# Optimization experiments

Hardware: AMD Instinct MI355X
Metric: run time of the kernel (lower is better)

The kernel has to match this reference:

```python
import jax, jax.numpy as jnp
import numpy as np

B, T_ENC, T_DEC = 32, 600, 600
TARGET, PRE, HID, ATT, LOCF, LOCK, POSTH = 80, 256, 512, 128, 32, 31, 512


def _lstm(x, h, c, wih, whh, bih, bhh):
    g = x @ wih.T + bih + h @ whh.T + bhh
    i, f, gg, o = jnp.split(g, 4, axis=-1)
    c2 = jax.nn.sigmoid(f) * c + jax.nn.sigmoid(i) * jnp.tanh(gg)
    return jax.nn.sigmoid(o) * jnp.tanh(c2), c2


def _conv1d(x, w, pad):
    return jax.lax.conv_general_dilated(x, w, (1,), [(pad, pad)], dimension_numbers=('NCH', 'OIH', 'NCH'))


def setup_inputs():
    key = jax.random.key(0)
    ks = jax.random.split(key, 24)
    rn = lambda k, s: jax.random.normal(k, s, dtype=jnp.float32) * 0.05
    return {
        'encoder_inputs': jax.random.normal(ks[0], (B, T_ENC, HID), dtype=jnp.float32),
        'decoder_inputs': jax.random.normal(ks[1], (B, T_DEC, TARGET), dtype=jnp.float32),
        'pn_w1': rn(ks[2], (PRE, TARGET)), 'pn_b1': jnp.zeros((PRE,), jnp.float32),
        'pn_w2': rn(ks[3], (PRE, PRE)), 'pn_b2': jnp.zeros((PRE,), jnp.float32),
        'arnn_wih': rn(ks[4], (4 * HID, PRE + HID)), 'arnn_whh': rn(ks[5], (4 * HID, HID)),
        'arnn_bih': jnp.zeros((4 * HID,), jnp.float32), 'arnn_bhh': jnp.zeros((4 * HID,), jnp.float32),
        'drnn_wih': rn(ks[6], (4 * HID, 2 * HID)), 'drnn_whh': rn(ks[7], (4 * HID, HID)),
        'drnn_bih': jnp.zeros((4 * HID,), jnp.float32), 'drnn_bhh': jnp.zeros((4 * HID,), jnp.float32),
        'mem_w': rn(ks[8], (ATT, HID)), 'mem_b': jnp.zeros((ATT,), jnp.float32),
        'q_w': rn(ks[9], (ATT, HID)),
        'loc_conv_w': rn(ks[10], (LOCF, 2, LOCK)),
        'loc_fc_w': rn(ks[11], (ATT, LOCF)),
        'v_w': rn(ks[12], (1, ATT)),
        'proj_w': rn(ks[13], (TARGET, 2 * HID)),
        'post_w0': rn(ks[14], (POSTH, TARGET, 5)), 'post_b0': jnp.zeros((POSTH,), jnp.float32),
        'post_w1': rn(ks[15], (POSTH, POSTH, 5)), 'post_b1': jnp.zeros((POSTH,), jnp.float32),
        'post_w2': rn(ks[16], (POSTH, POSTH, 5)), 'post_b2': jnp.zeros((POSTH,), jnp.float32),
        'post_w3': rn(ks[17], (POSTH, POSTH, 5)), 'post_b3': jnp.zeros((POSTH,), jnp.float32),
        'post_w4': rn(ks[18], (TARGET, POSTH, 5)), 'post_b4': jnp.zeros((TARGET,), jnp.float32),
    }


def _forward(encoder_inputs, decoder_inputs, pn_w1, pn_b1, pn_w2, pn_b2,
             arnn_wih, arnn_whh, arnn_bih, arnn_bhh,
             drnn_wih, drnn_whh, drnn_bih, drnn_bhh,
             mem_w, mem_b, q_w, loc_conv_w, loc_fc_w, v_w, proj_w,
             post_w0, post_b0, post_w1, post_b1, post_w2, post_b2,
             post_w3, post_b3, post_w4, post_b4):
    Bsz, Tdec, tdim = decoder_inputs.shape
    Tenc = encoder_inputs.shape[1]
    dt = decoder_inputs.dtype
    # prenet on [go_frame; decoder_inputs]; loop consumes frames 0..Tdec-1
    go = jnp.zeros((Bsz, 1, tdim), dt)
    dec = jnp.concatenate([go, decoder_inputs], axis=1)
    pre = jax.nn.relu(jax.nn.relu(dec @ pn_w1.T + pn_b1) @ pn_w2.T + pn_b2)
    xs = jnp.transpose(pre[:, :Tdec], (1, 0, 2))  # (Tdec, B, PRE)
    proc_mem = encoder_inputs @ mem_w.T + mem_b  # (B, Tenc, ATT)
    z = jnp.zeros((Bsz, HID), dt)
    zw = jnp.zeros((Bsz, Tenc), dt)
    carry0 = (z, z, z, z, z, zw, zw)

    def step(carry, dec_in):
        ah, ac, dh, dc, ctx, w, wcum = carry
        ah, ac = _lstm(jnp.concatenate([dec_in, ctx], -1), ah, ac, arnn_wih, arnn_whh, arnn_bih, arnn_bhh)
        wcat = jnp.stack([w, wcum], axis=1)  # (B, 2, Tenc)
        loc = _conv1d(wcat, loc_conv_w, (LOCK - 1) // 2)  # (B, LOCF, Tenc)
        loc = jnp.einsum('bct,ac->bta', loc, loc_fc_w)  # (B, Tenc, ATT)
        q = ah @ q_w.T  # (B, ATT)
        e = jnp.tanh(q[:, None, :] + proc_mem + loc) @ v_w[0]  # (B, Tenc)
        w2 = jax.nn.softmax(e, axis=-1)
        ctx2 = jnp.einsum('bt,bte->be', w2, encoder_inputs)
        wcum2 = wcum + w2
        dh2, dc2 = _lstm(jnp.concatenate([ah, ctx2], -1), dh, dc, drnn_wih, drnn_whh, drnn_bih, drnn_bhh)
        mel = jnp.concatenate([dh2, ctx2], -1) @ proj_w.T  # (B, TARGET)
        return (ah, ac, dh2, dc2, ctx2, w2, wcum2), mel

    _, mels = jax.lax.scan(step, carry0, xs)
    mel_out = jnp.transpose(mels, (1, 0, 2))  # (B, Tdec, TARGET)
    # postnet: 5 conv1d layers, tanh on all but last (eval mode, no dropout)
    y = jnp.transpose(mel_out, (0, 2, 1))  # (B, TARGET, Tdec)
    y = jnp.tanh(_conv1d(y, post_w0, 2) + post_b0[None, :, None])
    y = jnp.tanh(_conv1d(y, post_w1, 2) + post_b1[None, :, None])
    y = jnp.tanh(_conv1d(y, post_w2, 2) + post_b2[None, :, None])
    y = jnp.tanh(_conv1d(y, post_w3, 2) + post_b3[None, :, None])
    y = _conv1d(y, post_w4, 2) + post_b4[None, :, None]  # (B, TARGET, Tdec)
    return mel_out + jnp.transpose(y, (0, 2, 1))


def reference(encoder_inputs, decoder_inputs, pn_w1, pn_b1, pn_w2, pn_b2,
              arnn_wih, arnn_whh, arnn_bih, arnn_bhh,
              drnn_wih, drnn_whh, drnn_bih, drnn_bhh,
              mem_w, mem_b, q_w, loc_conv_w, loc_fc_w, v_w, proj_w,
              post_w0, post_b0, post_w1, post_b1, post_w2, post_b2,
              post_w3, post_b3, post_w4, post_b4):
    return _forward(encoder_inputs, decoder_inputs, pn_w1, pn_b1, pn_w2, pn_b2,
                    arnn_wih, arnn_whh, arnn_bih, arnn_bhh,
                    drnn_wih, drnn_whh, drnn_bih, drnn_bhh,
                    mem_w, mem_b, q_w, loc_conv_w, loc_fc_w, v_w, proj_w,
                    post_w0, post_b0, post_w1, post_b1, post_w2, post_b2,
                    post_w3, post_b3, post_w4, post_b4)
```

## Files before the change

kernel.cpp:

```cpp
#include <hip/hip_runtime.h>
#include <hip/hip_bf16.h>

typedef __hip_bfloat16 bf16;

#define NB   32
#define TE   600
#define TD   600
#define TGT  80
#define PREN 256
#define HID  512
#define ATTD 128
#define LF   32
#define LK   31
#define PH   512

__device__ __forceinline__ float b2f(bf16 x){ return __bfloat162float(x); }

__device__ __forceinline__ void ld8bf(const bf16* p, float* o){
  const uint4 u = *(const uint4*)p;
  o[0]=__uint_as_float(u.x<<16); o[1]=__uint_as_float(u.x&0xFFFF0000u);
  o[2]=__uint_as_float(u.y<<16); o[3]=__uint_as_float(u.y&0xFFFF0000u);
  o[4]=__uint_as_float(u.z<<16); o[5]=__uint_as_float(u.z&0xFFFF0000u);
  o[6]=__uint_as_float(u.w<<16); o[7]=__uint_as_float(u.w&0xFFFF0000u);
}

__device__ __forceinline__ void ld8f(const float* p, float* o){
  float4 a=*(const float4*)p, b=*(const float4*)(p+4);
  o[0]=a.x;o[1]=a.y;o[2]=a.z;o[3]=a.w;
  o[4]=b.x;o[5]=b.y;o[6]=b.z;o[7]=b.w;
}

__device__ __forceinline__ float dot8(const float* w, const float* z){
  return w[0]*z[0]+w[1]*z[1]+w[2]*z[2]+w[3]*z[3]
       + w[4]*z[4]+w[5]*z[5]+w[6]*z[6]+w[7]*z[7];
}

__device__ __forceinline__ float sigm(float x){ return 1.f/(1.f+__expf(-x)); }
__device__ __forceinline__ float tanhfast(float x){
  float e = __expf(2.f*x);
  return 1.f - 2.f/(e+1.f);
}

__global__ __launch_bounds__(256) void k_prenet(const float* __restrict__ dec,
    const float* __restrict__ w1, const float* __restrict__ b1,
    const float* __restrict__ w2, const float* __restrict__ b2,
    bf16* __restrict__ XS)
{
  int t = blockIdx.x, tid = threadIdx.x;
  __shared__ __align__(16) float fr[NB*TGT];
  __shared__ __align__(16) float h1[NB*PREN];
  for (int i=tid;i<NB*TGT;i+=256){
    int b=i/TGT,c=i%TGT;
    fr[b*TGT+c] = (t==0)?0.f:dec[((size_t)b*TD+(t-1))*TGT+c];
  }
  __syncthreads();
  {
    int oc=tid; float bb=b1[oc];
    const float* wr = w1 + (size_t)oc*TGT;
    for (int b=0;b<NB;b++){
      float acc=bb;
      for (int k=0;k<TGT;k+=8){
        float wv[8]; ld8f(wr+k,wv);
        acc += dot8(wv, fr + b*TGT + k);
      }
      h1[b*PREN+oc]=fmaxf(acc,0.f);
    }
  }
  __syncthreads();
  {
    int oc=tid; float bb=b2[oc];
    const float* wr = w2 + (size_t)oc*PREN;
    for (int b=0;b<NB;b++){
      float acc=bb;
      for (int k=0;k<PREN;k+=8){
        float wv[8]; ld8f(wr+k,wv);
        acc += dot8(wv, h1 + b*PREN + k);
      }
      XS[((size_t)t*NB+b)*PREN+oc]=__float2bfloat16(fmaxf(acc,0.f));
    }
  }
}

__global__ __launch_bounds__(256) void k_procmem(const float* __restrict__ enc,
    const float* __restrict__ mw, const float* __restrict__ mb, bf16* __restrict__ PM)
{
  int t=blockIdx.x, tid=threadIdx.x;
  __shared__ __align__(16) float xe[16*HID];
  int a = tid & 127, bh = tid >> 7;
  float bb = mb[a];
  const float* wr = mw + (size_t)a*HID;
  for (int half=0; half<2; half++){
    __syncthreads();
    for (int i=tid;i<16*HID;i+=256){
      int bl=i>>9, h=i&511;
      xe[i] = enc[((size_t)(half*16+bl)*TE + t)*HID + h];
    }
    __syncthreads();
    for (int bl=bh*8; bl<bh*8+8; bl++){
      float acc=bb;
      for (int k=0;k<HID;k+=8){
        float wv[8]; ld8f(wr+k,wv);
        acc += dot8(wv, xe + bl*HID + k);
      }
      PM[((size_t)(half*16+bl)*TE + t)*ATTD + a] = __float2bfloat16(acc);
    }
  }
}

__global__ __launch_bounds__(256) void k_bc(
    const float* __restrict__ AH, const bf16* __restrict__ PML,
    const float* __restrict__ enc,
    const float* __restrict__ qw, const float* __restrict__ vw,
    float* __restrict__ W, float* __restrict__ WCUM, float* __restrict__ CTXw,
    const float* __restrict__ DHp, const float* __restrict__ CTXp,
    const float* __restrict__ projw, float* __restrict__ MEL, int t)
{
  int blk=blockIdx.x, tid=threadIdx.x;
  if (blk>=128){
    if (t==0) return;
    int b = blk-128;
    const float* dh = DHp + b*HID;
    const float* c2 = CTXp + b*HID;
    #pragma unroll
    for (int pass=0; pass<3; ++pass){
      int o = pass*32 + (tid>>3);
      if (o<TGT){
        int j = tid&7;
        const float* pw = projw + (size_t)o*1024;
        float a=0.f;
        for (int i=0;i<16;i++){
          int k = j*128 + i*8;
          const float* zp = (k<512)? dh+k : c2+(k-512);
          float z[8]; ld8f(zp,z);
          float wv[8]; ld8f(pw+k,wv);
          a += dot8(wv,z);
        }
        a += __shfl_xor(a,1); a += __shfl_xor(a,2); a += __shfl_xor(a,4);
        if (j==0) MEL[((size_t)b*TD + (t-1))*TGT + o] = a;
      }
    }
    return;
  }
  int b = blk>>2, k4 = blk&3;
  __shared__ float qs[128], vv[128];
  __shared__ __align__(16) float el[608], wl[608];
  __shared__ __align__(16) float4 part4[256];
  __shared__ float red[4];
  if (tid < 128){
    vv[tid] = vw[tid];
    const float* qr = qw + (size_t)tid*HID;
    const float* ah = AH + b*HID;
    float acc = 0.f;
    for (int kk=0;kk<HID;kk+=8){
      float wv2[8]; ld8f(qr+kk,wv2);
      acc += dot8(wv2, ah+kk);
    }
    qs[tid] = acc;
  }
  __syncthreads();
  for (int r=0;r<3;r++){
    int tt=tid+r*256;
    if (tt<TE){
      const uint4* pm4=(const uint4*)(PML+((size_t)b*TE+tt)*ATTD);
      float s=0.f;
      #pragma unroll 4
      for (int g=0;g<16;g++){
        uint4 um=pm4[g];
        unsigned mm[4]={um.x,um.y,um.z,um.w};
        #pragma unroll
        for (int q=0;q<4;q++){
          int a=g*8+q*2;
          float x0=qs[a]  +__uint_as_float(mm[q]<<16);
          float x1=qs[a+1]+__uint_as_float(mm[q]&0xFFFF0000u);
          s+=vv[a]*tanhfast(x0)+vv[a+1]*tanhfast(x1);
        }
      }
      el[tt]=s;
    }
  }
  __syncthreads();
  float e0[3]; float mx=-1e30f;
  #pragma unroll
  for (int r=0;r<3;r++){
    int i=tid+r*256;
    float v=(i<TE)? el[i] : -1e30f;
    e0[r]=v; mx=fmaxf(mx,v);
  }
  for (int off=1;off<64;off<<=1) mx=fmaxf(mx,__shfl_xor(mx,off));
  if ((tid&63)==0) red[tid>>6]=mx;
  __syncthreads();
  float m=fmaxf(fmaxf(red[0],red[1]),fmaxf(red[2],red[3]));
  float ex[3]; float s=0.f;
  #pragma unroll
  for (int r=0;r<3;r++){
    int i=tid+r*256;
    ex[r]=(i<TE)? __expf(e0[r]-m) : 0.f;
    s+=ex[r];
  }
  for (int off=1;off<64;off<<=1) s+=__shfl_xor(s,off);
  __syncthreads();
  if ((tid&63)==0) red[tid>>6]=s;
  __syncthreads();
  float inv=1.f/(red[0]+red[1]+red[2]+red[3]);
  #pragma unroll
  for (int r=0;r<3;r++){
    int i=tid+r*256;
    if (i<TE){
      float w2=ex[r]*inv;
      wl[i]=w2;
      if (k4==0){
        W[(size_t)b*TE+i]=w2;
        WCUM[(size_t)b*TE+i]+=w2;
      }
    }
  }
  __syncthreads();
  {
    int hl = tid&31, tl = tid>>5;
    int h = k4*128 + hl*4;
    const float4* ep4 = (const float4*)(enc + ((size_t)b*TE)*HID + h);
    float4 acc; acc.x=0.f; acc.y=0.f; acc.z=0.f; acc.w=0.f;
    for (int u=0; u<75; ++u){
      int tt = tl + u*8;
      float w = wl[tt];
      float4 e = ep4[(size_t)tt*(HID/4)];
      acc.x += w*e.x; acc.y += w*e.y; acc.z += w*e.z; acc.w += w*e.w;
    }
    part4[tid]=acc;
  }
  __syncthreads();
  if (tid<32){
    float4 s4; s4.x=0.f; s4.y=0.f; s4.z=0.f; s4.w=0.f;
    #pragma unroll
    for (int k=0;k<8;k++){
      float4 p = part4[k*32+tid];
      s4.x+=p.x; s4.y+=p.y; s4.z+=p.z; s4.w+=p.w;
    }
    *(float4*)(CTXw + b*HID + k4*128 + tid*4) = s4;
  }
}

__global__ __launch_bounds__(256) void k_ea(
    const bf16* __restrict__ XS,
    const float* __restrict__ CTXt, const float* __restrict__ AHt,
    float* __restrict__ AHw, float* __restrict__ AC,
    const float* __restrict__ DHp, float* __restrict__ DHw, float* __restrict__ DC,
    const float* __restrict__ W, const float* __restrict__ WCUM,
    const float* __restrict__ convw, const float* __restrict__ fcw,
    const bf16* __restrict__ PM, bf16* __restrict__ PML,
    const float* __restrict__ awih, const float* __restrict__ awhh,
    const float* __restrict__ abih, const float* __restrict__ abhh,
    const float* __restrict__ dwih, const float* __restrict__ dwhh,
    const float* __restrict__ dbih, const float* __restrict__ dbhh,
    int t)
{
  int blk=blockIdx.x, tid=threadIdx.x;
  if (blk<512){
    int s = t+1;
    if (s>=TD) return;
    int b=tid>>3, j=tid&7;
    int cell = blk;
    const bf16* xs = XS + ((size_t)s*NB+b)*PREN;
    const float* cx = CTXt + b*HID;
    const float* hr = AHt + b*HID;
    float acc[4];
    #pragma unroll
    for (int q=0;q<4;q++) acc[q]=0.f;
    for (int i=0;i<20;i++){
      int k8=i*64+j*8;
      float z[8];
      if (k8<256) ld8bf(xs+k8,z);
      else ld8f((k8<768)? cx+(k8-256) : hr+(k8-768), z);
      #pragma unroll
      for (int g=0;g<4;g++){
        int row = g*HID + cell;
        const float* wp = (k8<768) ? (awih + (size_t)row*768 + k8)
                                   : (awhh + (size_t)row*HID + (k8-768));
        float wv[8]; ld8f(wp,wv);
        acc[g] += dot8(wv,z);
      }
    }
    #pragma unroll
    for (int q=0;q<4;q++){
      acc[q] += __shfl_xor(acc[q],1);
      acc[q] += __shfl_xor(acc[q],2);
      acc[q] += __shfl_xor(acc[q],4);
    }
    if (j==0){
      float g0=acc[0]+abih[0*HID+cell]+abhh[0*HID+cell];
      float g1=acc[1]+abih[1*HID+cell]+abhh[1*HID+cell];
      float g2=acc[2]+abih[2*HID+cell]+abhh[2*HID+cell];
      float g3=acc[3]+abih[3*HID+cell]+abhh[3*HID+cell];
      float c2 = sigm(g1)*AC[b*HID+cell] + sigm(g0)*tanhfast(g2);
      AC[b*HID+cell]=c2;
      AHw[b*HID+cell]=sigm(g3)*tanhfast(c2);
    }
  } else if (blk<1024){
    if (t<0) return;
    int b=tid>>3, j=tid&7;
    int cell = blk-512;
    const float* ah  = AHt + b*HID;
    const float* cx  = CTXt + b*HID;
    const float* dhr = DHp + b*HID;
    float acc[4];
    #pragma unroll
    for (int q=0;q<4;q++) acc[q]=0.f;
    for (int i=0;i<24;i++){
      int k8=i*64+j*8;
      const float* zp = (k8<512)? ah+k8 : (k8<1024)? cx+(k8-512) : dhr+(k8-1024);
      float z[8]; ld8f(zp,z);
      #pragma unroll
      for (int g=0;g<4;g++){
        int row = g*HID + cell;
        const float* wp = (k8<1024) ? (dwih + (size_t)row*1024 + k8)
                                    : (dwhh + (size_t)row*HID + (k8-1024));
        float wv[8]; ld8f(wp,wv);
        acc[g] += dot8(wv,z);
      }
    }
    #pragma unroll
    for (int q=0;q<4;q++){
      acc[q] += __shfl_xor(acc[q],1);
      acc[q] += __shfl_xor(acc[q],2);
      acc[q] += __shfl_xor(acc[q],4);
    }
    if (j==0){
      float g0=acc[0]+dbih[0*HID+cell]+dbhh[0*HID+cell];
      float g1=acc[1]+dbih[1*HID+cell]+dbhh[1*HID+cell];
      float g2=acc[2]+dbih[2*HID+cell]+dbhh[2*HID+cell];
      float g3=acc[3]+dbih[3*HID+cell]+dbhh[3*HID+cell];
      float c2 = sigm(g1)*DC[b*HID+cell] + sigm(g0)*tanhfast(g2);
      DC[b*HID+cell]=c2;
      DHw[b*HID+cell]=sigm(g3)*tanhfast(c2);
    }
  } else {
    if (t+1>=TD) return;
    int idx = blk-1024;
    int b = idx>>3, s8 = idx&7;
    int tb = s8*75;
    __shared__ __align__(16) float wp_[112], wc_[112];
    __shared__ __align__(16) float cw0[32*31], cw1[32*31];
    __shared__ __align__(16) float cb[75*32];
    __shared__ __align__(16) float fcs[128*33];
    if (tid<105){
      int g = tb-15+tid;
      bool ok = (g>=0 && g<TE);
      wp_[tid] = ok ? W[(size_t)b*TE+g] : 0.f;
      wc_[tid] = ok ? WCUM[(size_t)b*TE+g] : 0.f;
    }
    for (int i=tid;i<32*31;i+=256){
      int c=i/31, k=i-c*31;
      cw0[i] = convw[c*62 + k];
      cw1[i] = convw[c*62 + 31 + k];
    }
    for (int i=tid;i<128*33;i+=256){
      int a=i/33, c=i-a*33;
      fcs[i] = (c<32)? fcw[a*32+c] : 0.f;
    }
    __syncthreads();
    for (int i=tid;i<75*32;i+=256){
      int tt=i>>5, c=i&31;
      float s=0.f;
      for (int k=0;k<LK;k++)
        s += cw0[c*31+k]*wp_[tt+k] + cw1[c*31+k]*wc_[tt+k];
      cb[tt*32+c]=s;
    }
    __syncthreads();
    {
      int lane = tid&63, tl = tid>>6;
      int a0 = 2*lane;
      for (int tt=tl; tt<75; tt+=4){
        float l0=0.f, l1=0.f;
        const float* cbr = cb + tt*32;
        #pragma unroll
        for (int c=0;c<32;c++){
          float cv = cbr[c];
          l0 += fcs[a0*33+c]*cv;
          l1 += fcs[(a0+1)*33+c]*cv;
        }
        size_t off = ((size_t)b*TE + tb + tt)*ATTD + a0;
        PML[off]   = __float2bfloat16(l0 + b2f(PM[off]));
        PML[off+1] = __float2bfloat16(l1 + b2f(PM[off+1]));
      }
    }
  }
}

__global__ __launch_bounds__(256) void k_melfinal(const float* __restrict__ DH,
    const float* __restrict__ CTX, const float* __restrict__ projw, float* __restrict__ MEL)
{
  int gid=blockIdx.x*256+threadIdx.x;
  if (gid>=NB*TGT) return;
  int o=gid%TGT, b=gid/TGT;
  const float* pw=projw+(size_t)o*1024;
  float a=0.f;
  for (int k=0;k<HID;k+=8){
    float wv[8]; ld8f(pw+k,wv);
    a += dot8(wv, DH + b*HID + k);
  }
  for (int k=0;k<HID;k+=8){
    float wv[8]; ld8f(pw+512+k,wv);
    a += dot8(wv, CTX + b*HID + k);
  }
  MEL[((size_t)b*TD+599)*TGT+o]=a;
}

__global__ __launch_bounds__(256) void k_conv(
    const void* __restrict__ inv_, bf16* __restrict__ out,
    const float* __restrict__ w, const float* __restrict__ bias,
    int IC, int OC, int mel_in, int do_tanh, int b0)
{
  __shared__ __align__(16) float xs[256*36];
  int bl=blockIdx.x, bg=b0+bl, oct=blockIdx.y, t0=blockIdx.z*32, tid=threadIdx.x;
  int oc = oct*256 + tid;
  float acc[32];
  #pragma unroll
  for (int q=0;q<32;q++) acc[q]=0.f;
  int nch=(IC+255)/256;
  const float* inf_ = (const float*)inv_;
  const bf16*  inb_ = (const bf16*)inv_;
  for (int ch=0;ch<nch;ch++){
    int icb=ch*256, icn=min(256,IC-icb);
    __syncthreads();
    for (int i=tid;i<icn*36;i+=256){
      int icl=i/36, tt=i-icl*36;
      int tg=t0+tt-2;
      float v=0.f;
      if (tg>=0 && tg<TD){
        int ic=icb+icl;
        v = mel_in ? inf_[((size_t)bg*TD+tg)*TGT+ic]
                   : b2f(inb_[((size_t)bl*IC+ic)*TD+tg]);
      }
      xs[i]=v;
    }
    __syncthreads();
    if (oc<OC){
      const float* wp = w + ((size_t)oc*IC+icb)*5;
      for (int ic=0;ic<icn;ic++){
        float xw[36];
        #pragma unroll
        for (int q=0;q<9;q++) ((float4*)xw)[q]=((const float4*)(xs+ic*36))[q];
        float wk0=wp[ic*5  ],wk1=wp[ic*5+1],wk2=wp[ic*5+2],
              wk3=wp[ic*5+3],wk4=wp[ic*5+4];
        #pragma unroll
        for (int tt=0;tt<32;tt++)
          acc[tt] += wk0*xw[tt]+wk1*xw[tt+1]+wk2*xw[tt+2]+wk3*xw[tt+3]+wk4*xw[tt+4];
      }
    }
  }
  if (oc<OC){
    float bv=bias[oc];
    for (int tt=0;tt<32;tt++){
      int tg=t0+tt;
      if (tg<TD){
        float v=acc[tt]+bv;
        if (do_tanh) v=tanhfast(v);
        out[((size_t)bl*OC+oc)*TD+tg]=__float2bfloat16(v);
      }
    }
  }
}

__global__ __launch_bounds__(256) void k_conv_last(
    const bf16* __restrict__ in, const float* __restrict__ w,
    const float* __restrict__ bias, float* __restrict__ outp, int b0)
{
  __shared__ __align__(16) float xs[256*36];
  int bl=blockIdx.x, bg=b0+bl, t0=blockIdx.z*32, tid=threadIdx.x;
  int oc = tid;
  float acc[32];
  #pragma unroll
  for (int q=0;q<32;q++) acc[q]=0.f;
  for (int ch=0;ch<2;ch++){
    int icb=ch*256;
    __syncthreads();
    for (int i=tid;i<256*36;i+=256){
      int icl=i/36, tt=i-icl*36;
      int tg=t0+tt-2;
      float v=0.f;
      if (tg>=0 && tg<TD){
        int ic=icb+icl;
        v = b2f(in[((size_t)bl*PH+ic)*TD+tg]);
      }
      xs[i]=v;
    }
    __syncthreads();
    if (oc<TGT){
      const float* wp = w + ((size_t)oc*PH+icb)*5;
      for (int ic=0;ic<256;ic++){
        float xw[36];
        #pragma unroll
        for (int q=0;q<9;q++) ((float4*)xw)[q]=((const float4*)(xs+ic*36))[q];
        float wk0=wp[ic*5  ],wk1=wp[ic*5+1],wk2=wp[ic*5+2],
              wk3=wp[ic*5+3],wk4=wp[ic*5+4];
        #pragma unroll
        for (int tt=0;tt<32;tt++)
          acc[tt] += wk0*xw[tt]+wk1*xw[tt+1]+wk2*xw[tt+2]+wk3*xw[tt+3]+wk4*xw[tt+4];
      }
    }
  }
  if (oc<TGT){
    float bv=bias[oc];
    for (int tt=0;tt<32;tt++){
      int tg=t0+tt;
      if (tg<TD){
        size_t idx=((size_t)bg*TD+tg)*TGT+oc;
        outp[idx]=acc[tt]+bv+outp[idx];
      }
    }
  }
}

extern "C" void kernel_launch(void* const* d_in, const int* in_sizes, int n_in,
                              void* d_out, int out_size, void* d_ws, size_t ws_size,
                              hipStream_t stream)
{
  const float* enc =(const float*)d_in[0];
  const float* dec =(const float*)d_in[1];
  const float* pw1 =(const float*)d_in[2];  const float* pb1=(const float*)d_in[3];
  const float* pw2 =(const float*)d_in[4];  const float* pb2=(const float*)d_in[5];
  const float* awih=(const float*)d_in[6];  const float* awhh=(const float*)d_in[7];
  const float* abih=(const float*)d_in[8];  const float* abhh=(const float*)d_in[9];
  const float* dwih=(const float*)d_in[10]; const float* dwhh=(const float*)d_in[11];
  const float* dbih=(const float*)d_in[12]; const float* dbhh=(const float*)d_in[13];
  const float* memw=(const float*)d_in[14]; const float* memb=(const float*)d_in[15];
  const float* qw  =(const float*)d_in[16];
  const float* lcw =(const float*)d_in[17];
  const float* lfw =(const float*)d_in[18];
  const float* vw  =(const float*)d_in[19];
  const float* pjw =(const float*)d_in[20];
  const float* cwt0=(const float*)d_in[21]; const float* cbt0=(const float*)d_in[22];
  const float* cwt1=(const float*)d_in[23]; const float* cbt1=(const float*)d_in[24];
  const float* cwt2=(const float*)d_in[25]; const float* cbt2=(const float*)d_in[26];
  const float* cwt3=(const float*)d_in[27]; const float* cbt3=(const float*)d_in[28];
  const float* cwt4=(const float*)d_in[29]; const float* cbt4=(const float*)d_in[30];
  float* MEL = (float*)d_out;
  (void)in_sizes; (void)n_in; (void)out_size; (void)ws_size;

  char* base=(char*)d_ws;
  const size_t XS_B = (size_t)TD*NB*PREN*2;
  const size_t PM_B = (size_t)NB*TE*ATTD*2;
  const size_t HB   = (size_t)NB*HID*4;
  const size_t WB   = (size_t)NB*TE*4;
  bf16* XSb = (bf16*)base;
  bf16* PMb = (bf16*)(base + XS_B);
  char* sbase = base + XS_B + PM_B;
  float* AHb[2], *DHb[2], *CTXb[2];
  AHb[0] =(float*)(sbase+0*HB);
  AHb[1] =(float*)(sbase+1*HB);
  float* ACb =(float*)(sbase+2*HB);
  DHb[0] =(float*)(sbase+3*HB);
  DHb[1] =(float*)(sbase+4*HB);
  float* DCb =(float*)(sbase+5*HB);
  CTXb[0]=(float*)(sbase+6*HB);
  CTXb[1]=(float*)(sbase+7*HB);
  float* Wb  =(float*)(sbase+8*HB);
  float* WC  =(float*)(sbase+8*HB+WB);
  bf16*  PMLb=(bf16*)(sbase+8*HB+2*WB);
  const int G = 8;
  const size_t PBc_B = (size_t)G*PH*TD*2;
  bf16* PB0 = (bf16*)base;
  bf16* PB1 = (bf16*)(base + PBc_B);

  hipMemsetAsync(sbase, 0, 8*HB+2*WB, stream);

  k_prenet<<<TD,256,0,stream>>>(dec,pw1,pb1,pw2,pb2,XSb);
  k_procmem<<<TE,256,0,stream>>>(enc,memw,memb,PMb);

  k_ea<<<1280,256,0,stream>>>(XSb, CTXb[1], AHb[1], AHb[0], ACb,
                              DHb[0], DHb[1], DCb, Wb, WC, lcw, lfw, PMb, PMLb,
                              awih,awhh,abih,abhh,dwih,dwhh,dbih,dbhh, -1);
  for (int t=0;t<TD;t++){
    float* AHt  = AHb[t&1];
    float* AHw  = AHb[(t+1)&1];
    float* DHp  = DHb[(t+1)&1];
    float* DHw  = DHb[t&1];
    float* CTXt = CTXb[t&1];
    float* CTXp = CTXb[(t+1)&1];
    k_bc<<<160,256,0,stream>>>(AHt, PMLb, enc, qw, vw,
                               Wb, WC, CTXt, DHp, CTXp, pjw, MEL, t);
    k_ea<<<1280,256,0,stream>>>(XSb, CTXt, AHt, AHw, ACb,
                                DHp, DHw, DCb, Wb, WC, lcw, lfw, PMb, PMLb,
                                awih,awhh,abih,abhh,dwih,dwhh,dbih,dbhh, t);
  }
  k_melfinal<<<10,256,0,stream>>>(DHb[1],CTXb[1],pjw,MEL);

  for (int c=0;c<NB/G;c++){
    int b0=c*G;
    k_conv<<<dim3(G,2,19),256,0,stream>>>(MEL,PB0,cwt0,cbt0,TGT,PH,1,1,b0);
    k_conv<<<dim3(G,2,19),256,0,stream>>>(PB0,PB1,cwt1,cbt1,PH,PH,0,1,b0);
    k_conv<<<dim3(G,2,19),256,0,stream>>>(PB1,PB0,cwt2,cbt2,PH,PH,0,1,b0);
    k_conv<<<dim3(G,2,19),256,0,stream>>>(PB0,PB1,cwt3,cbt3,PH,PH,0,1,b0);
    k_conv_last<<<dim3(G,1,19),256,0,stream>>>(PB1,cwt4,cbt4,MEL,b0);
  }
}
```

Baseline: 59.21 ms.

## Use bf16 copy of encoder for attention context and reshape k_bc to 512-thread blocks

Converts encoder inputs to a bf16 copy once up front, when workspace is large enough, and reads that copy in the per-step attention-context reduction, halving its memory traffic. k_bc is restructured into 2 blocks of 512 threads per batch instead of 4 blocks of 256, and the query projection is split across 4 threads per output with a shuffle reduction. This recomputes the scores and softmax half as many times per batch but adds a bf16 rounding error to the context vector. It also adds one extra conversion kernel.

```diff
diff --git a/kernel.cpp b/kernel.cpp
--- a/kernel.cpp
+++ b/kernel.cpp
@@ -41,6 +41,20 @@
   return 1.f - 2.f/(e+1.f);
 }
 
+__global__ __launch_bounds__(256) void k_e2b(const float* __restrict__ s,
+    bf16* __restrict__ d, int n)
+{
+  int i=(blockIdx.x*256+threadIdx.x)*4;
+  int stride=gridDim.x*256*4;
+  for (; i<n; i+=stride){
+    float4 v=*(const float4*)(s+i);
+    d[i  ]=__float2bfloat16(v.x);
+    d[i+1]=__float2bfloat16(v.y);
+    d[i+2]=__float2bfloat16(v.z);
+    d[i+3]=__float2bfloat16(v.w);
+  }
+}
+
 __global__ __launch_bounds__(256) void k_prenet(const float* __restrict__ dec,
     const float* __restrict__ w1, const float* __restrict__ b1,
     const float* __restrict__ w2, const float* __restrict__ b2,
@@ -107,18 +121,19 @@
   }
 }
 
-__global__ __launch_bounds__(256) void k_bc(
+template<int EB>
+__global__ __launch_bounds__(512) void k_bc(
     const float* __restrict__ AH, const bf16* __restrict__ PML,
-    const float* __restrict__ enc,
+    const float* __restrict__ enc, const bf16* __restrict__ encb,
     const float* __restrict__ qw, const float* __restrict__ vw,
     float* __restrict__ W, float* __restrict__ WCUM, float* __restrict__ CTXw,
     const float* __restrict__ DHp, const float* __restrict__ CTXp,
     const float* __restrict__ projw, float* __restrict__ MEL, int t)
 {
   int blk=blockIdx.x, tid=threadIdx.x;
-  if (blk>=128){
-    if (t==0) return;
-    int b = blk-128;
+  if (blk>=64){
+    if (t==0 || tid>=256) return;
+    int b = blk-64;
     const float* dh = DHp + b*HID;
     const float* c2 = CTXp + b*HID;
     #pragma unroll
@@ -141,25 +156,28 @@
     }
     return;
   }
-  int b = blk>>2, k4 = blk&3;
+  int b = blk>>1, k2 = blk&1;
   __shared__ float qs[128], vv[128];
   __shared__ __align__(16) float el[608], wl[608];
-  __shared__ __align__(16) float4 part4[256];
-  __shared__ float red[4];
-  if (tid < 128){
-    vv[tid] = vw[tid];
-    const float* qr = qw + (size_t)tid*HID;
-    const float* ah = AH + b*HID;
+  __shared__ __align__(16) float part[4096];
+  __shared__ float red[8];
+  {
+    if (tid<128) vv[tid]=vw[tid];
+    int a = tid>>2, kl = tid&3;
+    const float* qr = qw + (size_t)a*HID + kl*128;
+    const float* ah = AH + b*HID + kl*128;
     float acc = 0.f;
-    for (int kk=0;kk<HID;kk+=8){
-      float wv2[8]; ld8f(qr+kk,wv2);
-      acc += dot8(wv2, ah+kk);
-    }
-    qs[tid] = acc;
-  }
-  __syncthreads();
-  for (int r=0;r<3;r++){
-    int tt=tid+r*256;
+    for (int i=0;i<16;i++){
+      float wv2[8]; ld8f(qr+i*8,wv2);
+      acc += dot8(wv2, ah+i*8);
+    }
+    acc += __shfl_xor(acc,1);
+    acc += __shfl_xor(acc,2);
+    if (kl==0) qs[a]=acc;
+  }
+  __syncthreads();
+  for (int r=0;r<2;r++){
+    int tt=tid+r*512;
     if (tt<TE){
       const uint4* pm4=(const uint4*)(PML+((size_t)b*TE+tt)*ATTD);
       float s=0.f;
@@ -179,21 +197,23 @@
     }
   }
   __syncthreads();
-  float e0[3]; float mx=-1e30f;
+  float e0[2]; float mx=-1e30f;
   #pragma unroll
-  for (int r=0;r<3;r++){
-    int i=tid+r*256;
+  for (int r=0;r<2;r++){
+    int i=tid+r*512;
     float v=(i<TE)? el[i] : -1e30f;
     e0[r]=v; mx=fmaxf(mx,v);
   }
   for (int off=1;off<64;off<<=1) mx=fmaxf(mx,__shfl_xor(mx,off));
   if ((tid&63)==0) red[tid>>6]=mx;
   __syncthreads();
-  float m=fmaxf(fmaxf(red[0],red[1]),fmaxf(red[2],red[3]));
-  float ex[3]; float s=0.f;
+  float m=-1e30f;
   #pragma unroll
-  for (int r=0;r<3;r++){
-    int i=tid+r*256;
+  for (int k=0;k<8;k++) m=fmaxf(m,red[k]);
+  float ex[2]; float s=0.f;
+  #pragma unroll
+  for (int r=0;r<2;r++){
+    int i=tid+r*512;
     ex[r]=(i<TE)? __expf(e0[r]-m) : 0.f;
     s+=ex[r];
   }
@@ -201,42 +221,65 @@
   __syncthreads();
   if ((tid&63)==0) red[tid>>6]=s;
   __syncthreads();
-  float inv=1.f/(red[0]+red[1]+red[2]+red[3]);
+  float sum=0.f;
   #pragma unroll
-  for (int r=0;r<3;r++){
-    int i=tid+r*256;
+  for (int k=0;k<8;k++) sum+=red[k];
+  float inv=1.f/sum;
+  #pragma unroll
+  for (int r=0;r<2;r++){
+    int i=tid+r*512;
     if (i<TE){
       float w2=ex[r]*inv;
       wl[i]=w2;
-      if (k4==0){
+      if (k2==0){
         W[(size_t)b*TE+i]=w2;
         WCUM[(size_t)b*TE+i]+=w2;
       }
     }
   }
   __syncthreads();
-  {
-    int hl = tid&31, tl = tid>>5;
-    int h = k4*128 + hl*4;
-    const float4* ep4 = (const float4*)(enc + ((size_t)b*TE)*HID + h);
+  if (EB){
+    int g = tid&31, tl = tid>>5;
+    const bf16* ep = encb + ((size_t)b*TE)*HID + k2*256 + g*8;
+    float acc[8];
+    #pragma unroll
+    for (int e=0;e<8;e++) acc[e]=0.f;
+    for (int u=0;u<38;u++){
+      int tt = tl + u*16;
+      if (tt<TE){
+        float w = wl[tt];
+        float z[8]; ld8bf(ep + (size_t)tt*HID, z);
+        #pragma unroll
+        for (int e=0;e<8;e++) acc[e] += w*z[e];
+      }
+    }
+    #pragma unroll
+    for (int e=0;e<8;e++) part[tid*8+e]=acc[e];
+  } else {
+    int g = tid&63, tl = tid>>6;
+    const float4* ep4 = (const float4*)(enc + ((size_t)b*TE)*HID + k2*256 + g*4);
     float4 acc; acc.x=0.f; acc.y=0.f; acc.z=0.f; acc.w=0.f;
-    for (int u=0; u<75; ++u){
+    for (int u=0;u<75;u++){
       int tt = tl + u*8;
       float w = wl[tt];
       float4 e = ep4[(size_t)tt*(HID/4)];
       acc.x += w*e.x; acc.y += w*e.y; acc.z += w*e.z; acc.w += w*e.w;
     }
-    part4[tid]=acc;
-  }
-  __syncthreads();
-  if (tid<32){
-    float4 s4; s4.x=0.f; s4.y=0.f; s4.z=0.f; s4.w=0.f;
-    #pragma unroll
-    for (int k=0;k<8;k++){
-      float4 p = part4[k*32+tid];
-      s4.x+=p.x; s4.y+=p.y; s4.z+=p.z; s4.w+=p.w;
-    }
-    *(float4*)(CTXw + b*HID + k4*128 + tid*4) = s4;
+    ((float4*)part)[tid]=acc;
+  }
+  __syncthreads();
+  if (tid<256){
+    float sH=0.f;
+    if (EB){
+      int gh = tid>>3, e = tid&7;
+      #pragma unroll
+      for (int tl=0;tl<16;tl++) sH += part[(tl*32+gh)*8 + e];
+    } else {
+      int gh = tid>>2, e = tid&3;
+      #pragma unroll
+      for (int tl=0;tl<8;tl++) sH += part[(tl*64+gh)*4 + e];
+    }
+    CTXw[b*HID + k2*256 + tid] = sH;
   }
 }
 
@@ -535,7 +578,7 @@
   const float* cwt3=(const float*)d_in[27]; const float* cbt3=(const float*)d_in[28];
   const float* cwt4=(const float*)d_in[29]; const float* cbt4=(const float*)d_in[30];
   float* MEL = (float*)d_out;
-  (void)in_sizes; (void)n_in; (void)out_size; (void)ws_size;
+  (void)in_sizes; (void)n_in; (void)out_size;
 
   char* base=(char*)d_ws;
   const size_t XS_B = (size_t)TD*NB*PREN*2;
@@ -557,6 +600,11 @@
   float* Wb  =(float*)(sbase+8*HB);
   float* WC  =(float*)(sbase+8*HB+WB);
   bf16*  PMLb=(bf16*)(sbase+8*HB+2*WB);
+  const size_t BASE_B = XS_B + PM_B + 8*HB + 2*WB + PM_B;
+  bf16* ENCB = (bf16*)(base + BASE_B);
+  const size_t ENC_B = (size_t)NB*TE*HID*2;
+  const bool useE = (ws_size >= BASE_B + ENC_B);
+
   const int G = 8;
   const size_t PBc_B = (size_t)G*PH*TD*2;
   bf16* PB0 = (bf16*)base;
@@ -564,6 +612,7 @@
 
   hipMemsetAsync(sbase, 0, 8*HB+2*WB, stream);
 
+  if (useE) k_e2b<<<2048,256,0,stream>>>(enc, ENCB, NB*TE*HID);
   k_prenet<<<TD,256,0,stream>>>(dec,pw1,pb1,pw2,pb2,XSb);
   k_procmem<<<TE,256,0,stream>>>(enc,memw,memb,PMb);
 
@@ -577,8 +626,12 @@
     float* DHw  = DHb[t&1];
     float* CTXt = CTXb[t&1];
     float* CTXp = CTXb[(t+1)&1];
-    k_bc<<<160,256,0,stream>>>(AHt, PMLb, enc, qw, vw,
-                               Wb, WC, CTXt, DHp, CTXp, pjw, MEL, t);
+    if (useE)
+      k_bc<1><<<96,512,0,stream>>>(AHt, PMLb, enc, ENCB, qw, vw,
+                                   Wb, WC, CTXt, DHp, CTXp, pjw, MEL, t);
+    else
+      k_bc<0><<<96,512,0,stream>>>(AHt, PMLb, enc, ENCB, qw, vw,
+                                   Wb, WC, CTXt, DHp, CTXp, pjw, MEL, t);
     k_ea<<<1280,256,0,stream>>>(XSb, CTXt, AHt, AHw, ACb,
                                 DHp, DHw, DCb, Wb, WC, lcw, lfw, PMb, PMLb,
                                 awih,awhh,abih,abhh,dwih,dwhh,dbih,dbhh, t);
```

Measured after the change: 58.28 ms. About the same (-1.6%).
